# Performance work log

Hardware: AMD Instinct MI355X
Metric: run time of the kernel (lower is better)

Reference implementation:

```python
import jax, jax.numpy as jnp
import numpy as np

NEG_SLOPE = 0.01  # torch LeakyReLU default

def setup_inputs() -> dict:
    key = jax.random.key(0)
    ks = jax.random.split(key, 8)
    B, T, D = 8, 2048, 512
    E, H = 8, 2 * D  # n_experts, ffn hidden
    s = 0.02
    return {
        "x":  jax.random.normal(ks[0], (B, T, D), dtype=jnp.float32),
        "Wr": jax.random.normal(ks[1], (D, E), dtype=jnp.float32) * s,
        "br": jnp.zeros((E,), dtype=jnp.float32),
        "W1": jax.random.normal(ks[2], (E, D, H), dtype=jnp.float32) * s,
        "b1": jnp.zeros((E, H), dtype=jnp.float32),
        "W2": jax.random.normal(ks[3], (E, H, D), dtype=jnp.float32) * s,
        "b2": jnp.zeros((E, D), dtype=jnp.float32),
    }

def reference(x, Wr, br, W1, b1, W2, b2):
    B, T, D = x.shape
    E = Wr.shape[1]
    top_k = 2
    balancing_coef = 1e-4
    x_flat = x.reshape(B * T, D)  # [N, D]

    # router: softmax over experts
    router_probs = jax.nn.softmax(x_flat @ Wr + br, axis=-1)  # [N, E]
    top_weights, top_indices = jax.lax.top_k(router_probs, top_k)  # [N, k]

    # dense all-expert FFN (faithful to original: every expert on every token)
    h = jax.nn.leaky_relu(jnp.einsum('nd,edh->neh', x_flat, W1) + b1, NEG_SLOPE)  # [N, E, H]
    expert_out = jax.nn.leaky_relu(jnp.einsum('neh,ehd->ned', h, W2) + b2, NEG_SLOPE)  # [N, E, D]
    # dropout is identity in eval mode

    # gather top-k expert outputs and combine with router weights
    top_out = jnp.take_along_axis(expert_out, top_indices[:, :, None], axis=1)  # [N, k, D]
    out_flat = jnp.sum(top_out * top_weights[:, :, None], axis=1)  # [N, D]
    output = out_flat.reshape(B, T, D)

    # load-balancing loss
    target = jnp.full((E,), 1.0 / E, dtype=x.dtype)
    mean_probs = jnp.mean(router_probs, axis=0)
    gating_loss = jnp.mean((target - mean_probs) ** 2) * balancing_coef
    return (output, gating_loss)
```

## Files before the change

kernel.cpp:

```cpp
#include <hip/hip_runtime.h>
#include <hip/hip_bf16.h>

constexpr int D_    = 512;
constexpr int H_    = 1024;
constexpr int E_    = 8;
constexpr int NTOK_ = 16384;
constexpr int MT_   = 64;
constexpr int NPAIR_= 2*NTOK_;
constexpr float NEG_ = 0.01f;

typedef short s16x8 __attribute__((ext_vector_type(8)));
typedef float f32x4 __attribute__((ext_vector_type(4)));

#define MFMA16(a,b,c) __builtin_amdgcn_mfma_f32_16x16x32_bf16((a),(b),(c),0,0,0)

__device__ __forceinline__ unsigned short f2bf(float f) {
  unsigned u = __float_as_uint(f);
  u += 0x7FFFu + ((u >> 16) & 1u);
  return (unsigned short)(u >> 16);
}
__device__ __forceinline__ float bf2f(unsigned u16) {
  return __uint_as_float(u16 << 16);
}
__device__ __forceinline__ float leaky(float v) {
  return v > 0.f ? v : NEG_ * v;
}

__global__ __launch_bounds__(256) void convert_kernel(
    const float* __restrict__ W1, const float* __restrict__ W2,
    unsigned short* __restrict__ W1s, unsigned short* __restrict__ W2s) {
  int gid = blockIdx.x * 256 + threadIdx.x;
  const int HALF = E_ * 64 * 16 * 64;
  if (gid < HALF) {
    int lane = gid & 63, kk = (gid >> 6) & 15, nt = (gid >> 10) & 63, e = gid >> 16;
    int k0 = kk * 32 + (lane >> 4) * 8;
    int n  = nt * 16 + (lane & 15);
    const float* src = W1 + ((size_t)(e * 512 + k0)) * 1024 + n;
    s16x8 v;
#pragma unroll
    for (int j = 0; j < 8; j++) v[j] = (short)f2bf(src[(size_t)j * 1024]);
    *(s16x8*)(W1s + (size_t)gid * 8) = v;
  } else {
    int c = gid - HALF;
    int lane = c & 63, kk = (c >> 6) & 31, nt = (c >> 11) & 31, e = c >> 16;
    int k0 = kk * 32 + (lane >> 4) * 8;
    int n  = nt * 16 + (lane & 15);
    const float* src = W2 + ((size_t)(e * 1024 + k0)) * 512 + n;
    s16x8 v;
#pragma unroll
    for (int j = 0; j < 8; j++) v[j] = (short)f2bf(src[(size_t)j * 512]);
    *(s16x8*)(W2s + (size_t)c * 8) = v;
  }
}

__global__ __launch_bounds__(256) void router_kernel(
    const float* __restrict__ x, const float* __restrict__ Wr,
    const float* __restrict__ br,
    int* __restrict__ cnt, float* __restrict__ psum,
    int* __restrict__ tokE, int* __restrict__ tokSlot, float* __restrict__ tokW) {
  __shared__ int lcnt[E_];
  __shared__ int gbase[E_];
  __shared__ float lp[E_];
  int tid = threadIdx.x;
  if (tid < E_) { lcnt[tid] = 0; lp[tid] = 0.f; }
  __syncthreads();

  int t = blockIdx.x * 256 + tid;
  float acc[E_];
#pragma unroll
  for (int e = 0; e < E_; e++) acc[e] = br[e];
  const float4* xr = (const float4*)(x + (size_t)t * D_);
  for (int i = 0; i < D_ / 4; i++) {
    float4 v = xr[i];
    const float* w = Wr + (size_t)i * 4 * E_;
#pragma unroll
    for (int e = 0; e < E_; e++)
      acc[e] += v.x * w[e] + v.y * w[8 + e] + v.z * w[16 + e] + v.w * w[24 + e];
  }
  float mx = acc[0];
#pragma unroll
  for (int e = 1; e < E_; e++) mx = fmaxf(mx, acc[e]);
  float p[E_]; float s = 0.f;
#pragma unroll
  for (int e = 0; e < E_; e++) { p[e] = expf(acc[e] - mx); s += p[e]; }
  float inv = 1.f / s;
#pragma unroll
  for (int e = 0; e < E_; e++) p[e] *= inv;

  float m1 = -1.f, m2 = -1.f; int i1 = 0, i2 = 0;
#pragma unroll
  for (int e = 0; e < E_; e++) {
    float pe = p[e];
    if (pe > m1)      { m2 = m1; i2 = i1; m1 = pe; i1 = e; }
    else if (pe > m2) { m2 = pe; i2 = e; }
  }
  int s1 = atomicAdd(&lcnt[i1], 1);
  int s2 = atomicAdd(&lcnt[i2], 1);

#pragma unroll
  for (int e = 0; e < E_; e++) {
    float v = p[e];
#pragma unroll
    for (int o = 32; o > 0; o >>= 1) v += __shfl_xor(v, o);
    if ((tid & 63) == 0) atomicAdd(&lp[e], v);
  }
  __syncthreads();
  if (tid < E_) {
    gbase[tid] = atomicAdd(&cnt[tid * 16], lcnt[tid]);
    atomicAdd(&psum[tid * 16], lp[tid]);
  }
  __syncthreads();
  tokE[2 * t]     = i1; tokSlot[2 * t]     = gbase[i1] + s1; tokW[2 * t]     = m1;
  tokE[2 * t + 1] = i2; tokSlot[2 * t + 1] = gbase[i2] + s2; tokW[2 * t + 1] = m2;
}

__global__ void scan_kernel(const int* __restrict__ cnt, int* __restrict__ off,
                            const float* __restrict__ psum, float* __restrict__ loss_out) {
  if (threadIdx.x == 0) {
    int o = 0;
    for (int e = 0; e < E_; e++) { off[e] = o; o += cnt[e * 16]; }
    float l = 0.f;
    for (int e = 0; e < E_; e++) {
      float d = 0.125f - psum[e * 16] / (float)NTOK_;
      l += d * d;
    }
    *loss_out = (l / 8.f) * 1e-4f;
  }
}

__global__ __launch_bounds__(256) void assign_kernel(
    const int* __restrict__ tokE, const int* __restrict__ tokSlot,
    const int* __restrict__ off,
    int* __restrict__ posOfTok, int* __restrict__ tokOfPos) {
  int p = blockIdx.x * 256 + threadIdx.x;
  if (p >= NPAIR_) return;
  int pos = off[tokE[p]] + tokSlot[p];
  posOfTok[p] = pos;
  tokOfPos[pos] = p >> 1;
}

__global__ __launch_bounds__(512, 2) void ffn_kernel(
    const float* __restrict__ x,
    const unsigned short* __restrict__ W1s, const unsigned short* __restrict__ W2s,
    const float* __restrict__ b1, const float* __restrict__ b2,
    const int* __restrict__ cnt, const int* __restrict__ off,
    const int* __restrict__ tokOfPos, unsigned short* __restrict__ buf) {
  const int e = blockIdx.x & 7;
  const int tile = blockIdx.x >> 3;
  const int nTok = cnt[e * 16];
  const int start = tile * MT_;
  if (start >= nTok) return;
  const int valid = min(MT_, nTok - start);
  const int base = off[e] + start;

  __shared__ __align__(16) unsigned short xs[MT_][D_ + 8];
  __shared__ __align__(16) unsigned short hs[2][MT_][136];
  __shared__ int toks[MT_];

  const int tid = threadIdx.x;
  const int w = tid >> 6;
  const int lane = tid & 63;

  if (tid < MT_) toks[tid] = tokOfPos[base + min(tid, valid - 1)];
  __syncthreads();

  for (int r = w; r < MT_; r += 8) {
    const float4* src = (const float4*)(x + (size_t)toks[r] * D_);
    float4 a = src[lane * 2], b = src[lane * 2 + 1];
    s16x8 v;
    v[0] = (short)f2bf(a.x); v[1] = (short)f2bf(a.y);
    v[2] = (short)f2bf(a.z); v[3] = (short)f2bf(a.w);
    v[4] = (short)f2bf(b.x); v[5] = (short)f2bf(b.y);
    v[6] = (short)f2bf(b.z); v[7] = (short)f2bf(b.w);
    *(s16x8*)&xs[r][lane * 8] = v;
  }
  __syncthreads();

  const int qm = lane & 15;
  const int qk = (lane >> 4) * 8;
  const int qr = (lane >> 4) * 4;

  f32x4 acc2[4][4];
#pragma unroll
  for (int mi = 0; mi < 4; mi++)
#pragma unroll
    for (int ni = 0; ni < 4; ni++) acc2[mi][ni] = {0.f, 0.f, 0.f, 0.f};

  for (int c = 0; c < 8; c++) {
    f32x4 acc1[4];
#pragma unroll
    for (int mi = 0; mi < 4; mi++) acc1[mi] = {0.f, 0.f, 0.f, 0.f};

    const unsigned short* B1base =
        W1s + ((size_t)(e * 64 + c * 8 + w) * 16) * 512 + lane * 8;
#pragma unroll 4
    for (int kk = 0; kk < 16; kk++) {
      s16x8 b = *(const s16x8*)(B1base + (size_t)kk * 512);
#pragma unroll
      for (int mi = 0; mi < 4; mi++) {
        s16x8 a = *(const s16x8*)&xs[mi * 16 + qm][kk * 32 + qk];
        acc1[mi] = MFMA16(a, b, acc1[mi]);
      }
    }
    {
      int hcol = w * 16 + qm;
      float bb = b1[e * H_ + c * 128 + hcol];
#pragma unroll
      for (int mi = 0; mi < 4; mi++)
#pragma unroll
        for (int r4 = 0; r4 < 4; r4++)
          hs[c & 1][mi * 16 + qr + r4][hcol] = f2bf(leaky(acc1[mi][r4] + bb));
    }
    __syncthreads();
    const unsigned short* B2base =
        W2s + ((size_t)(e * 32) * 32) * 512 + lane * 8;
#pragma unroll
    for (int kk = 0; kk < 4; kk++) {
      s16x8 a[4];
#pragma unroll
      for (int mi = 0; mi < 4; mi++)
        a[mi] = *(const s16x8*)&hs[c & 1][mi * 16 + qm][kk * 32 + qk];
#pragma unroll
      for (int ni = 0; ni < 4; ni++) {
        s16x8 bb = *(const s16x8*)(B2base +
            (size_t)((w * 4 + ni) * 32 + c * 4 + kk) * 512);
#pragma unroll
        for (int mi = 0; mi < 4; mi++) acc2[mi][ni] = MFMA16(a[mi], bb, acc2[mi][ni]);
      }
    }
  }

#pragma unroll
  for (int mi = 0; mi < 4; mi++) {
#pragma unroll
    for (int r4 = 0; r4 < 4; r4++) {
      int row = mi * 16 + qr + r4;
      if (row < valid) {
        size_t rowbase = (size_t)(base + row) * D_;
#pragma unroll
        for (int ni = 0; ni < 4; ni++) {
          int col = w * 64 + ni * 16 + qm;
          float v = leaky(acc2[mi][ni][r4] + b2[e * D_ + col]);
          buf[rowbase + col] = f2bf(v);
        }
      }
    }
  }
}

__global__ __launch_bounds__(256) void combine_kernel(
    const unsigned short* __restrict__ buf, const int* __restrict__ posOfTok,
    const float* __restrict__ tokW, float* __restrict__ out) {
  int t = blockIdx.x;
  int tid = threadIdx.x;
  int p0 = posOfTok[2 * t], p1 = posOfTok[2 * t + 1];
  float w0 = tokW[2 * t], w1 = tokW[2 * t + 1];
  const unsigned* r0 = (const unsigned*)(buf + (size_t)p0 * D_);
  const unsigned* r1 = (const unsigned*)(buf + (size_t)p1 * D_);
  unsigned u0 = r0[tid], u1 = r1[tid];
  float2 o;
  o.x = w0 * bf2f(u0 & 0xFFFFu) + w1 * bf2f(u1 & 0xFFFFu);
  o.y = w0 * bf2f(u0 >> 16)     + w1 * bf2f(u1 >> 16);
  ((float2*)(out + (size_t)t * D_))[tid] = o;
}

extern "C" void kernel_launch(void* const* d_in, const int* in_sizes, int n_in,
                              void* d_out, int out_size, void* d_ws, size_t ws_size,
                              hipStream_t stream) {
  const float* x  = (const float*)d_in[0];
  const float* Wr = (const float*)d_in[1];
  const float* br = (const float*)d_in[2];
  const float* W1 = (const float*)d_in[3];
  const float* b1 = (const float*)d_in[4];
  const float* W2 = (const float*)d_in[5];
  const float* b2 = (const float*)d_in[6];
  float* out = (float*)d_out;

  char* ws = (char*)d_ws;
  int*   cnt      = (int*)(ws + 0);
  float* psum     = (float*)(ws + 512);
  int*   off      = (int*)(ws + 1024);
  int*   tokE     = (int*)(ws + 4096);
  int*   tokSlot  = (int*)(ws + 4096 + 1 * 131072);
  float* tokW     = (float*)(ws + 4096 + 2 * 131072);
  int*   posOfTok = (int*)(ws + 4096 + 3 * 131072);
  int*   tokOfPos = (int*)(ws + 4096 + 4 * 131072);
  unsigned short* W1s = (unsigned short*)(ws + (1u << 20));
  unsigned short* W2s = (unsigned short*)(ws + (1u << 20) + 16777216u);
  unsigned short* buf = (unsigned short*)(ws + (1u << 20) + 33554432u);

  hipMemsetAsync(d_ws, 0, 2048, stream);
  convert_kernel<<<4096, 256, 0, stream>>>(W1, W2, W1s, W2s);
  router_kernel<<<NTOK_ / 256, 256, 0, stream>>>(x, Wr, br, cnt, psum,
                                                 tokE, tokSlot, tokW);
  scan_kernel<<<1, 64, 0, stream>>>(cnt, off, psum, out + (size_t)NTOK_ * D_);
  assign_kernel<<<NPAIR_ / 256, 256, 0, stream>>>(tokE, tokSlot, off,
                                                  posOfTok, tokOfPos);
  ffn_kernel<<<(NTOK_ / MT_) * E_, 512, 0, stream>>>(x, W1s, W2s, b1, b2,
                                                     cnt, off, tokOfPos, buf);
  combine_kernel<<<NTOK_, 256, 0, stream>>>(buf, posOfTok, tokW, out);
}
```

Before: 314.5 us.

## Merge prep kernels, retile FFN to 64x64 warp tiles, vectorize combine

Folds weight conversion and routing into a single prep kernel, and folds the offset scan and loss computation into the assign kernel, so there are fewer launches. The FFN kernel now runs the hidden dimension in two 512-wide chunks with a 4x4 MFMA tile per warp, using one larger shared buffer for h. This gives more reuse of each loaded B fragment and cuts the number of block barriers, at the cost of more shared memory and accumulator registers. The combine kernel now gives one wavefront per token and uses 16-byte loads and stores.

```diff
diff --git a/kernel.cpp b/kernel.cpp
--- a/kernel.cpp
+++ b/kernel.cpp
@@ -26,146 +26,153 @@
   return v > 0.f ? v : NEG_ * v;
 }
 
-__global__ __launch_bounds__(256) void convert_kernel(
-    const float* __restrict__ W1, const float* __restrict__ W2,
-    unsigned short* __restrict__ W1s, unsigned short* __restrict__ W2s) {
-  int gid = blockIdx.x * 256 + threadIdx.x;
-  const int HALF = E_ * 64 * 16 * 64;
-  if (gid < HALF) {
-    int lane = gid & 63, kk = (gid >> 6) & 15, nt = (gid >> 10) & 63, e = gid >> 16;
-    int k0 = kk * 32 + (lane >> 4) * 8;
-    int n  = nt * 16 + (lane & 15);
-    const float* src = W1 + ((size_t)(e * 512 + k0)) * 1024 + n;
-    s16x8 v;
-#pragma unroll
-    for (int j = 0; j < 8; j++) v[j] = (short)f2bf(src[(size_t)j * 1024]);
-    *(s16x8*)(W1s + (size_t)gid * 8) = v;
-  } else {
-    int c = gid - HALF;
-    int lane = c & 63, kk = (c >> 6) & 31, nt = (c >> 11) & 31, e = c >> 16;
-    int k0 = kk * 32 + (lane >> 4) * 8;
-    int n  = nt * 16 + (lane & 15);
-    const float* src = W2 + ((size_t)(e * 1024 + k0)) * 512 + n;
-    s16x8 v;
-#pragma unroll
-    for (int j = 0; j < 8; j++) v[j] = (short)f2bf(src[(size_t)j * 512]);
-    *(s16x8*)(W2s + (size_t)c * 8) = v;
-  }
-}
-
-__global__ __launch_bounds__(256) void router_kernel(
+__global__ __launch_bounds__(256) void prep_kernel(
     const float* __restrict__ x, const float* __restrict__ Wr,
     const float* __restrict__ br,
+    const float* __restrict__ W1, const float* __restrict__ W2,
+    unsigned short* __restrict__ W1s, unsigned short* __restrict__ W2s,
     int* __restrict__ cnt, float* __restrict__ psum,
     int* __restrict__ tokE, int* __restrict__ tokSlot, float* __restrict__ tokW) {
-  __shared__ int lcnt[E_];
-  __shared__ int gbase[E_];
-  __shared__ float lp[E_];
+  const int blk = blockIdx.x;
+  const int tid = threadIdx.x;
+  if (blk < 64) {
+    __shared__ int lcnt[E_];
+    __shared__ int gbase[E_];
+    __shared__ float lp[E_];
+    if (tid < E_) { lcnt[tid] = 0; lp[tid] = 0.f; }
+    __syncthreads();
+
+    int t = blk * 256 + tid;
+    float acc[E_];
+#pragma unroll
+    for (int e = 0; e < E_; e++) acc[e] = br[e];
+    const float4* xr = (const float4*)(x + (size_t)t * D_);
+    for (int i = 0; i < D_ / 4; i++) {
+      float4 v = xr[i];
+      const float* w = Wr + (size_t)i * 4 * E_;
+#pragma unroll
+      for (int e = 0; e < E_; e++)
+        acc[e] += v.x * w[e] + v.y * w[8 + e] + v.z * w[16 + e] + v.w * w[24 + e];
+    }
+    float mx = acc[0];
+#pragma unroll
+    for (int e = 1; e < E_; e++) mx = fmaxf(mx, acc[e]);
+    float p[E_]; float s = 0.f;
+#pragma unroll
+    for (int e = 0; e < E_; e++) { p[e] = expf(acc[e] - mx); s += p[e]; }
+    float inv = 1.f / s;
+#pragma unroll
+    for (int e = 0; e < E_; e++) p[e] *= inv;
+
+    float m1 = -1.f, m2 = -1.f; int i1 = 0, i2 = 0;
+#pragma unroll
+    for (int e = 0; e < E_; e++) {
+      float pe = p[e];
+      if (pe > m1)      { m2 = m1; i2 = i1; m1 = pe; i1 = e; }
+      else if (pe > m2) { m2 = pe; i2 = e; }
+    }
+    int s1 = atomicAdd(&lcnt[i1], 1);
+    int s2 = atomicAdd(&lcnt[i2], 1);
+
+#pragma unroll
+    for (int e = 0; e < E_; e++) {
+      float v = p[e];
+#pragma unroll
+      for (int o = 32; o > 0; o >>= 1) v += __shfl_xor(v, o);
+      if ((tid & 63) == 0) atomicAdd(&lp[e], v);
+    }
+    __syncthreads();
+    if (tid < E_) {
+      gbase[tid] = atomicAdd(&cnt[tid * 16], lcnt[tid]);
+      atomicAdd(&psum[tid * 16], lp[tid]);
+    }
+    __syncthreads();
+    tokE[2 * t]     = i1; tokSlot[2 * t]     = gbase[i1] + s1; tokW[2 * t]     = m1;
+    tokE[2 * t + 1] = i2; tokSlot[2 * t + 1] = gbase[i2] + s2; tokW[2 * t + 1] = m2;
+  } else {
+    int gid = (blk - 64) * 256 + tid;
+    const int HALF = E_ * 64 * 16 * 64;
+    if (gid < HALF) {
+      int lane = gid & 63, kk = (gid >> 6) & 15, nt = (gid >> 10) & 63, e = gid >> 16;
+      int k0 = kk * 32 + (lane >> 4) * 8;
+      int n  = nt * 16 + (lane & 15);
+      const float* src = W1 + ((size_t)(e * 512 + k0)) * 1024 + n;
+      s16x8 v;
+#pragma unroll
+      for (int j = 0; j < 8; j++) v[j] = (short)f2bf(src[(size_t)j * 1024]);
+      *(s16x8*)(W1s + (size_t)gid * 8) = v;
+    } else {
+      int c = gid - HALF;
+      int lane = c & 63, kk = (c >> 6) & 31, nt = (c >> 11) & 31, e = c >> 16;
+      int k0 = kk * 32 + (lane >> 4) * 8;
+      int n  = nt * 16 + (lane & 15);
+      const float* src = W2 + ((size_t)(e * 1024 + k0)) * 512 + n;
+      s16x8 v;
+#pragma unroll
+      for (int j = 0; j < 8; j++) v[j] = (short)f2bf(src[(size_t)j * 512]);
+      *(s16x8*)(W2s + (size_t)c * 8) = v;
+    }
+  }
+}
+
+__global__ __launch_bounds__(256) void assign_kernel(
+    const int* __restrict__ tokE, const int* __restrict__ tokSlot,
+    const int* __restrict__ cnt, const float* __restrict__ psum,
+    int* __restrict__ posOfTok, int* __restrict__ tokOfPos,
+    float* __restrict__ loss_out) {
+  __shared__ int soff[E_];
   int tid = threadIdx.x;
-  if (tid < E_) { lcnt[tid] = 0; lp[tid] = 0.f; }
+  if (tid == 0) {
+    int o = 0;
+#pragma unroll
+    for (int e = 0; e < E_; e++) { soff[e] = o; o += cnt[e * 16]; }
+  }
   __syncthreads();
-
-  int t = blockIdx.x * 256 + tid;
-  float acc[E_];
-#pragma unroll
-  for (int e = 0; e < E_; e++) acc[e] = br[e];
-  const float4* xr = (const float4*)(x + (size_t)t * D_);
-  for (int i = 0; i < D_ / 4; i++) {
-    float4 v = xr[i];
-    const float* w = Wr + (size_t)i * 4 * E_;
-#pragma unroll
-    for (int e = 0; e < E_; e++)
-      acc[e] += v.x * w[e] + v.y * w[8 + e] + v.z * w[16 + e] + v.w * w[24 + e];
-  }
-  float mx = acc[0];
-#pragma unroll
-  for (int e = 1; e < E_; e++) mx = fmaxf(mx, acc[e]);
-  float p[E_]; float s = 0.f;
-#pragma unroll
-  for (int e = 0; e < E_; e++) { p[e] = expf(acc[e] - mx); s += p[e]; }
-  float inv = 1.f / s;
-#pragma unroll
-  for (int e = 0; e < E_; e++) p[e] *= inv;
-
-  float m1 = -1.f, m2 = -1.f; int i1 = 0, i2 = 0;
-#pragma unroll
-  for (int e = 0; e < E_; e++) {
-    float pe = p[e];
-    if (pe > m1)      { m2 = m1; i2 = i1; m1 = pe; i1 = e; }
-    else if (pe > m2) { m2 = pe; i2 = e; }
-  }
-  int s1 = atomicAdd(&lcnt[i1], 1);
-  int s2 = atomicAdd(&lcnt[i2], 1);
-
-#pragma unroll
-  for (int e = 0; e < E_; e++) {
-    float v = p[e];
-#pragma unroll
-    for (int o = 32; o > 0; o >>= 1) v += __shfl_xor(v, o);
-    if ((tid & 63) == 0) atomicAdd(&lp[e], v);
-  }
-  __syncthreads();
-  if (tid < E_) {
-    gbase[tid] = atomicAdd(&cnt[tid * 16], lcnt[tid]);
-    atomicAdd(&psum[tid * 16], lp[tid]);
-  }
-  __syncthreads();
-  tokE[2 * t]     = i1; tokSlot[2 * t]     = gbase[i1] + s1; tokW[2 * t]     = m1;
-  tokE[2 * t + 1] = i2; tokSlot[2 * t + 1] = gbase[i2] + s2; tokW[2 * t + 1] = m2;
-}
-
-__global__ void scan_kernel(const int* __restrict__ cnt, int* __restrict__ off,
-                            const float* __restrict__ psum, float* __restrict__ loss_out) {
-  if (threadIdx.x == 0) {
-    int o = 0;
-    for (int e = 0; e < E_; e++) { off[e] = o; o += cnt[e * 16]; }
+  int p = blockIdx.x * 256 + tid;
+  int pos = soff[tokE[p]] + tokSlot[p];
+  posOfTok[p] = pos;
+  tokOfPos[pos] = p >> 1;
+  if (blockIdx.x == 0 && tid == 0) {
     float l = 0.f;
+#pragma unroll
     for (int e = 0; e < E_; e++) {
       float d = 0.125f - psum[e * 16] / (float)NTOK_;
       l += d * d;
     }
     *loss_out = (l / 8.f) * 1e-4f;
   }
-}
-
-__global__ __launch_bounds__(256) void assign_kernel(
-    const int* __restrict__ tokE, const int* __restrict__ tokSlot,
-    const int* __restrict__ off,
-    int* __restrict__ posOfTok, int* __restrict__ tokOfPos) {
-  int p = blockIdx.x * 256 + threadIdx.x;
-  if (p >= NPAIR_) return;
-  int pos = off[tokE[p]] + tokSlot[p];
-  posOfTok[p] = pos;
-  tokOfPos[pos] = p >> 1;
 }
 
 __global__ __launch_bounds__(512, 2) void ffn_kernel(
     const float* __restrict__ x,
     const unsigned short* __restrict__ W1s, const unsigned short* __restrict__ W2s,
     const float* __restrict__ b1, const float* __restrict__ b2,
-    const int* __restrict__ cnt, const int* __restrict__ off,
-    const int* __restrict__ tokOfPos, unsigned short* __restrict__ buf) {
+    const int* __restrict__ cnt, const int* __restrict__ tokOfPos,
+    unsigned short* __restrict__ buf) {
   const int e = blockIdx.x & 7;
   const int tile = blockIdx.x >> 3;
-  const int nTok = cnt[e * 16];
+  int nTok = 0, base0 = 0;
+#pragma unroll
+  for (int i = 0; i < E_; i++) {
+    int ci = cnt[i * 16];
+    if (i < e) base0 += ci;
+    if (i == e) nTok = ci;
+  }
   const int start = tile * MT_;
   if (start >= nTok) return;
   const int valid = min(MT_, nTok - start);
-  const int base = off[e] + start;
+  const int base = base0 + start;
 
   __shared__ __align__(16) unsigned short xs[MT_][D_ + 8];
-  __shared__ __align__(16) unsigned short hs[2][MT_][136];
-  __shared__ int toks[MT_];
+  __shared__ __align__(16) unsigned short hs[MT_][D_ + 8];
 
   const int tid = threadIdx.x;
   const int w = tid >> 6;
   const int lane = tid & 63;
 
-  if (tid < MT_) toks[tid] = tokOfPos[base + min(tid, valid - 1)];
-  __syncthreads();
-
   for (int r = w; r < MT_; r += 8) {
-    const float4* src = (const float4*)(x + (size_t)toks[r] * D_);
+    int tok = tokOfPos[base + min(r, valid - 1)];
+    const float4* src = (const float4*)(x + (size_t)tok * D_);
     float4 a = src[lane * 2], b = src[lane * 2 + 1];
     s16x8 v;
     v[0] = (short)f2bf(a.x); v[1] = (short)f2bf(a.y);
@@ -186,47 +193,59 @@
 #pragma unroll
     for (int ni = 0; ni < 4; ni++) acc2[mi][ni] = {0.f, 0.f, 0.f, 0.f};
 
-  for (int c = 0; c < 8; c++) {
-    f32x4 acc1[4];
-#pragma unroll
-    for (int mi = 0; mi < 4; mi++) acc1[mi] = {0.f, 0.f, 0.f, 0.f};
-
-    const unsigned short* B1base =
-        W1s + ((size_t)(e * 64 + c * 8 + w) * 16) * 512 + lane * 8;
+  const unsigned short* B1w = W1s + ((size_t)(e * 64 + w * 4) * 16) * 512 + lane * 8;
+  const unsigned short* B2w = W2s + ((size_t)(e * 32 + w * 4) * 32) * 512 + lane * 8;
+
+  for (int c = 0; c < 2; c++) {
+    f32x4 acc1[4][4];
+#pragma unroll
+    for (int mi = 0; mi < 4; mi++)
+#pragma unroll
+      for (int ni = 0; ni < 4; ni++) acc1[mi][ni] = {0.f, 0.f, 0.f, 0.f};
+
+    const unsigned short* B1c = B1w + (size_t)(c * 32 * 16) * 512;
 #pragma unroll 4
     for (int kk = 0; kk < 16; kk++) {
-      s16x8 b = *(const s16x8*)(B1base + (size_t)kk * 512);
-#pragma unroll
-      for (int mi = 0; mi < 4; mi++) {
-        s16x8 a = *(const s16x8*)&xs[mi * 16 + qm][kk * 32 + qk];
-        acc1[mi] = MFMA16(a, b, acc1[mi]);
-      }
-    }
-    {
-      int hcol = w * 16 + qm;
-      float bb = b1[e * H_ + c * 128 + hcol];
+      s16x8 bf[4], af[4];
+#pragma unroll
+      for (int ni = 0; ni < 4; ni++)
+        bf[ni] = *(const s16x8*)(B1c + (size_t)(ni * 16 + kk) * 512);
 #pragma unroll
       for (int mi = 0; mi < 4; mi++)
+        af[mi] = *(const s16x8*)&xs[mi * 16 + qm][kk * 32 + qk];
+#pragma unroll
+      for (int ni = 0; ni < 4; ni++)
+#pragma unroll
+        for (int mi = 0; mi < 4; mi++)
+          acc1[mi][ni] = MFMA16(af[mi], bf[ni], acc1[mi][ni]);
+    }
+    __syncthreads();
+#pragma unroll
+    for (int ni = 0; ni < 4; ni++) {
+      int hcol = w * 64 + ni * 16 + qm;
+      float bb = b1[e * H_ + c * 512 + hcol];
+#pragma unroll
+      for (int mi = 0; mi < 4; mi++)
 #pragma unroll
         for (int r4 = 0; r4 < 4; r4++)
-          hs[c & 1][mi * 16 + qr + r4][hcol] = f2bf(leaky(acc1[mi][r4] + bb));
-    }
-    __syncthreads();
-    const unsigned short* B2base =
-        W2s + ((size_t)(e * 32) * 32) * 512 + lane * 8;
-#pragma unroll
-    for (int kk = 0; kk < 4; kk++) {
-      s16x8 a[4];
+          hs[mi * 16 + qr + r4][hcol] = f2bf(leaky(acc1[mi][ni][r4] + bb));
+    }
+    __syncthreads();
+    const unsigned short* B2c = B2w + (size_t)(c * 16) * 512;
+#pragma unroll 4
+    for (int kk = 0; kk < 16; kk++) {
+      s16x8 bf[4], af[4];
+#pragma unroll
+      for (int ni = 0; ni < 4; ni++)
+        bf[ni] = *(const s16x8*)(B2c + (size_t)(ni * 32 + kk) * 512);
 #pragma unroll
       for (int mi = 0; mi < 4; mi++)
-        a[mi] = *(const s16x8*)&hs[c & 1][mi * 16 + qm][kk * 32 + qk];
-#pragma unroll
-      for (int ni = 0; ni < 4; ni++) {
-        s16x8 bb = *(const s16x8*)(B2base +
-            (size_t)((w * 4 + ni) * 32 + c * 4 + kk) * 512);
-#pragma unroll
-        for (int mi = 0; mi < 4; mi++) acc2[mi][ni] = MFMA16(a[mi], bb, acc2[mi][ni]);
-      }
+        af[mi] = *(const s16x8*)&hs[mi * 16 + qm][kk * 32 + qk];
+#pragma unroll
+      for (int ni = 0; ni < 4; ni++)
+#pragma unroll
+        for (int mi = 0; mi < 4; mi++)
+          acc2[mi][ni] = MFMA16(af[mi], bf[ni], acc2[mi][ni]);
     }
   }
 
@@ -251,17 +270,24 @@
 __global__ __launch_bounds__(256) void combine_kernel(
     const unsigned short* __restrict__ buf, const int* __restrict__ posOfTok,
     const float* __restrict__ tokW, float* __restrict__ out) {
-  int t = blockIdx.x;
-  int tid = threadIdx.x;
+  int t = blockIdx.x * 4 + (threadIdx.x >> 6);
+  int lane = threadIdx.x & 63;
   int p0 = posOfTok[2 * t], p1 = posOfTok[2 * t + 1];
   float w0 = tokW[2 * t], w1 = tokW[2 * t + 1];
-  const unsigned* r0 = (const unsigned*)(buf + (size_t)p0 * D_);
-  const unsigned* r1 = (const unsigned*)(buf + (size_t)p1 * D_);
-  unsigned u0 = r0[tid], u1 = r1[tid];
-  float2 o;
-  o.x = w0 * bf2f(u0 & 0xFFFFu) + w1 * bf2f(u1 & 0xFFFFu);
-  o.y = w0 * bf2f(u0 >> 16)     + w1 * bf2f(u1 >> 16);
-  ((float2*)(out + (size_t)t * D_))[tid] = o;
+  uint4 u0 = ((const uint4*)(buf + (size_t)p0 * D_))[lane];
+  uint4 u1 = ((const uint4*)(buf + (size_t)p1 * D_))[lane];
+  float4 oA, oB;
+  oA.x = w0 * bf2f(u0.x & 0xFFFFu) + w1 * bf2f(u1.x & 0xFFFFu);
+  oA.y = w0 * bf2f(u0.x >> 16)     + w1 * bf2f(u1.x >> 16);
+  oA.z = w0 * bf2f(u0.y & 0xFFFFu) + w1 * bf2f(u1.y & 0xFFFFu);
+  oA.w = w0 * bf2f(u0.y >> 16)     + w1 * bf2f(u1.y >> 16);
+  oB.x = w0 * bf2f(u0.z & 0xFFFFu) + w1 * bf2f(u1.z & 0xFFFFu);
+  oB.y = w0 * bf2f(u0.z >> 16)     + w1 * bf2f(u1.z >> 16);
+  oB.z = w0 * bf2f(u0.w & 0xFFFFu) + w1 * bf2f(u1.w & 0xFFFFu);
+  oB.w = w0 * bf2f(u0.w >> 16)     + w1 * bf2f(u1.w >> 16);
+  float4* dst = (float4*)(out + (size_t)t * D_);
+  dst[lane * 2]     = oA;
+  dst[lane * 2 + 1] = oB;
 }
 
 extern "C" void kernel_launch(void* const* d_in, const int* in_sizes, int n_in,
@@ -279,7 +305,6 @@
   char* ws = (char*)d_ws;
   int*   cnt      = (int*)(ws + 0);
   float* psum     = (float*)(ws + 512);
-  int*   off      = (int*)(ws + 1024);
   int*   tokE     = (int*)(ws + 4096);
   int*   tokSlot  = (int*)(ws + 4096 + 1 * 131072);
   float* tokW     = (float*)(ws + 4096 + 2 * 131072);
@@ -290,13 +315,12 @@
   unsigned short* buf = (unsigned short*)(ws + (1u << 20) + 33554432u);
 
   hipMemsetAsync(d_ws, 0, 2048, stream);
-  convert_kernel<<<4096, 256, 0, stream>>>(W1, W2, W1s, W2s);
-  router_kernel<<<NTOK_ / 256, 256, 0, stream>>>(x, Wr, br, cnt, psum,
-                                                 tokE, tokSlot, tokW);
-  scan_kernel<<<1, 64, 0, stream>>>(cnt, off, psum, out + (size_t)NTOK_ * D_);
-  assign_kernel<<<NPAIR_ / 256, 256, 0, stream>>>(tokE, tokSlot, off,
-                                                  posOfTok, tokOfPos);
+  prep_kernel<<<4160, 256, 0, stream>>>(x, Wr, br, W1, W2, W1s, W2s,
+                                        cnt, psum, tokE, tokSlot, tokW);
+  assign_kernel<<<NPAIR_ / 256, 256, 0, stream>>>(tokE, tokSlot, cnt, psum,
+                                                  posOfTok, tokOfPos,
+                                                  out + (size_t)NTOK_ * D_);
   ffn_kernel<<<(NTOK_ / MT_) * E_, 512, 0, stream>>>(x, W1s, W2s, b1, b2,
-                                                     cnt, off, tokOfPos, buf);
-  combine_kernel<<<NTOK_, 256, 0, stream>>>(buf, posOfTok, tokW, out);
-}
+                                                     cnt, tokOfPos, buf);
+  combine_kernel<<<NTOK_ / 4, 256, 0, stream>>>(buf, posOfTok, tokW, out);
+}
```

New measurement: 298.4 us. -5.1%, faster.
